# Kernel tuning notes

Measured on AMD Instinct MI355X. Metric: run time of the kernel, lower is better.

## Reference

```python
import jax, jax.numpy as jnp
import numpy as np

SEQ, BS, H, D = 2048, 2, 16, 64


def phi(x):
    # ELU(x / d**0.25) + 1
    return jax.nn.elu(x / (x.shape[-1] ** 0.25)) + 1.0


def setup_inputs() -> dict:
    key = jax.random.key(0)
    ks = jax.random.split(key, 5)
    return {
        "query_layer": jax.random.normal(ks[0], (SEQ, BS, H, D), jnp.float32),
        "key_layer": jax.random.normal(ks[1], (SEQ, BS, H, D), jnp.float32),
        "value_layer": jax.random.normal(ks[2], (SEQ, BS, H, D), jnp.float32),
        "attention_mask": jnp.zeros((BS, 1, SEQ, SEQ), dtype=bool),  # unused by forward
        "phi_k": jax.random.normal(ks[3], (1, H, D, 1), jnp.float32) / 10000.0,
        "phi_kv": jax.random.normal(ks[4], (1, H, D, D), jnp.float32) / 10000.0,
    }


def _ntk_attn(q, k, v, sum_phi_k, sum_phi_kv):
    # q,k,v: [bs,h,n,d]; sum_phi_k: [1,h,d,1]; sum_phi_kv: [1,h,d,d]
    d = q.shape[-1]
    nq, nk = q.shape[-2], k.shape[-2]
    kk = jnp.abs(sum_phi_k)
    Z = sum_phi_kv
    phi_q = phi(q)  # [bs,h,nq,d]
    A = jnp.einsum("bhqd,bhkd->bhqk", q, k) / jnp.sqrt(jnp.float32(d))
    max_A = jnp.max(A, axis=-1, keepdims=True)  # [bs,h,nq,1]
    exp_max_A = jnp.exp(max_A)
    A = jnp.exp(A - max_A)
    causal = jnp.tril(jnp.ones((nq, nk), jnp.float32), k=nk - nq)
    A = A * causal  # broadcast over [bs,h]
    D_norm = jnp.sum(A, axis=-1, keepdims=True) + jnp.matmul(phi_q, kk) / exp_max_A
    ctx = (jnp.matmul(A, v) + jnp.matmul(phi_q, Z) / exp_max_A) / D_norm
    return ctx  # [bs,h,nq,d]


def reference(query_layer, key_layer, value_layer, attention_mask, phi_k, phi_kv):
    # inputs are [seq, bs, h, d]; attention_mask is unused (module ignores it)
    q = jnp.transpose(query_layer, (1, 2, 0, 3)).astype(jnp.float32)
    k = jnp.transpose(key_layer, (1, 2, 0, 3)).astype(jnp.float32)
    v = jnp.transpose(value_layer, (1, 2, 0, 3)).astype(jnp.float32)
    ctx = _ntk_attn(q, k, v, phi_k, phi_kv)  # [bs,h,nq,d]
    ctx = jnp.transpose(ctx, (2, 0, 1, 3))  # [nq,bs,h,d]
    nq, bs, h, d = ctx.shape
    return ctx.reshape(nq, bs, h * d).astype(query_layer.dtype)
```

## Files before the change

### kernel.cpp

```cpp
#include <hip/hip_runtime.h>

#define SEQ 2048
#define BSZ 2
#define NHEAD 16
#define NBH (BSZ * NHEAD)
#define HDIM 64
#define QBLK 64
#define KVBLK 64
#define NQT (SEQ / QBLK)
#define ROWSTRIDE (BSZ * NHEAD * HDIM)

typedef __bf16 bf16x8 __attribute__((ext_vector_type(8)));
typedef __bf16 bf16x4 __attribute__((ext_vector_type(4)));
typedef float f32x4 __attribute__((ext_vector_type(4)));

#define AS1 __attribute__((address_space(1)))
#define AS3 __attribute__((address_space(3)))

__global__ __launch_bounds__(256)
void conv_all(const float* __restrict__ Kg, const float* __restrict__ Vg,
              const float* __restrict__ PKVg, __bf16* __restrict__ Kb,
              __bf16* __restrict__ Vt, __bf16* __restrict__ Ztb) {
  __shared__ __bf16 tt[HDIM][72];
  const int b = blockIdx.x;
  const int tid = threadIdx.x;

  if (b < 2048) {
    const int t = b * 256 + tid;
    const int s = t >> 8;
    const int bh = (t >> 3) & 31;
    const int d8 = (t & 7) * 8;
    const float* src = Kg + (size_t)s * ROWSTRIDE + bh * HDIM + d8;
    const float4 a = *(const float4*)src;
    const float4 bb = *(const float4*)(src + 4);
    bf16x8 o = {(__bf16)a.x, (__bf16)a.y, (__bf16)a.z, (__bf16)a.w,
                (__bf16)bb.x, (__bf16)bb.y, (__bf16)bb.z, (__bf16)bb.w};
    const int slot = (d8 >> 3) ^ (s & 7);
    *(bf16x8*)(Kb + ((size_t)bh * SEQ + s) * HDIM + slot * 8) = o;
  } else if (b < 3072) {
    const int t = b - 2048;
    const int kb = t & 31, bh = t >> 5;
    {
      const int r = tid >> 2, c16 = (tid & 3) * 16;
#pragma unroll
      for (int i = 0; i < 4; ++i) {
        const float4 v = *(const float4*)(Vg + (size_t)(kb * 64 + r) * ROWSTRIDE +
                                          bh * HDIM + c16 + 4 * i);
        tt[c16 + 4 * i + 0][r] = (__bf16)v.x;
        tt[c16 + 4 * i + 1][r] = (__bf16)v.y;
        tt[c16 + 4 * i + 2][r] = (__bf16)v.z;
        tt[c16 + 4 * i + 3][r] = (__bf16)v.w;
      }
    }
    __syncthreads();
    {
      const int d = tid >> 2, c2 = (tid & 3) * 2;
#pragma unroll
      for (int k8 = 0; k8 < 2; ++k8) {
        const int s8 = c2 + k8;
        const int pbase = (s8 ^ (d & 7)) * 8;
        __bf16 ov[8];
#pragma unroll
        for (int j = 0; j < 8; ++j) {
          const int p = pbase + j;
          const int P = p >> 5, g = (p >> 3) & 3, jj = p & 7;
          ov[j] = tt[d][32 * P + 16 * (jj >> 2) + 4 * g + (jj & 3)];
        }
        *(bf16x8*)(Vt + (((size_t)bh * 32 + kb) * 64 + d) * 64 + s8 * 8) =
            *(const bf16x8*)ov;
      }
    }
  } else {
    const int t = (b - 3072) * 256 + tid;
    const int lr = t & 15, lg = (t >> 4) & 3, c = (t >> 6) & 1;
    const int dj = (t >> 7) & 3, h = t >> 9;
    __bf16 o[8];
#pragma unroll
    for (int i = 0; i < 8; ++i)
      o[i] = (__bf16)PKVg[((size_t)h * 64 + 32 * c + 8 * lg + i) * 64 + dj * 16 + lr];
    *(bf16x8*)(Ztb + (size_t)t * 8) = *(const bf16x8*)o;
  }
}

__global__ __launch_bounds__(256, 4)
void ntk_attn(const float* __restrict__ Qg, const __bf16* __restrict__ Kb,
              const __bf16* __restrict__ Vt, const float* __restrict__ PKg,
              const __bf16* __restrict__ Ztb, float* __restrict__ Og) {
  __shared__ __bf16 Ks[2][KVBLK * HDIM];
  __shared__ __bf16 Vts[2][KVBLK * HDIM];

  const int tid = threadIdx.x;
  const int w = tid >> 6, l = tid & 63, lr = l & 15, lg = l >> 4;

  const int ord = blockIdx.x;
  const int bh = ord & 31, h = bh & (NHEAD - 1);
  const int v = ord >> 5;
  const int bx = (v < 16) ? v : 47 - v;
  const int q0 = bx * QBLK;
  const int ntile = bx + 1;
  const int headoff = bh * HDIM;
  const __bf16* Kbh = Kb + (size_t)bh * SEQ * HDIM;
  const __bf16* Vbh = Vt + (size_t)bh * SEQ * HDIM;

  auto stage = [&](int kb, int bb) {
    const char* gk = (const char*)Kbh + ((size_t)kb << 13) + (w << 11) + (l << 4);
    const char* gv = (const char*)Vbh + ((size_t)kb << 13) + (w << 11) + (l << 4);
    __bf16* lk = &Ks[bb][w << 10];
    __bf16* lv = &Vts[bb][w << 10];
    __builtin_amdgcn_global_load_lds((const AS1 unsigned*)gk,
                                     (AS3 unsigned*)lk, 16, 0, 0);
    __builtin_amdgcn_global_load_lds((const AS1 unsigned*)(gk + 1024),
                                     (AS3 unsigned*)(lk + 512), 16, 0, 0);
    __builtin_amdgcn_global_load_lds((const AS1 unsigned*)gv,
                                     (AS3 unsigned*)lv, 16, 0, 0);
    __builtin_amdgcn_global_load_lds((const AS1 unsigned*)(gv + 1024),
                                     (AS3 unsigned*)(lv + 512), 16, 0, 0);
  };

  stage(0, 0);

  bf16x8 aq[2], pq[2];
  {
    const float* qp = Qg + (size_t)(q0 + w * 16 + lr) * ROWSTRIDE + headoff + lg * 8;
#pragma unroll
    for (int c = 0; c < 2; ++c) {
      const float4 x0 = *(const float4*)(qp + 32 * c);
      const float4 x1 = *(const float4*)(qp + 32 * c + 4);
      const float f[8] = {x0.x, x0.y, x0.z, x0.w, x1.x, x1.y, x1.z, x1.w};
#pragma unroll
      for (int i = 0; i < 8; ++i) {
        aq[c][i] = (__bf16)(f[i] * 0.18033688011112042f);
        const float xs = f[i] * 0.3535533905932738f;
        pq[c][i] = (__bf16)(xs > 0.f ? xs + 1.f : __expf(xs));
      }
    }
  }

  const f32x4 z4 = {0.f, 0.f, 0.f, 0.f};
  f32x4 oacc[4] = {z4, z4, z4, z4};
  f32x4 dacc = z4;
  bf16x8 ones;
#pragma unroll
  for (int i = 0; i < 8; ++i) ones[i] = (__bf16)1.0f;
  const int qa = q0 + w * 16 + lr;
  const int sw = lr & 7;

  __syncthreads();
  int cur = 0;

  for (int kb = 0; kb < ntile; ++kb) {
    const bool more = (kb + 1 < ntile);
    if (more) stage(kb + 1, cur ^ 1);

    bf16x8 kc[4][2];
#pragma unroll
    for (int nj = 0; nj < 4; ++nj)
#pragma unroll
      for (int c = 0; c < 2; ++c)
        kc[nj][c] = *(const bf16x8*)&Ks[cur][(nj * 16 + lr) * 64 +
                                            (((4 * c + lg) ^ sw) << 3)];
    bf16x8 vv[2][4];
#pragma unroll
    for (int P = 0; P < 2; ++P)
#pragma unroll
      for (int dj = 0; dj < 4; ++dj)
        vv[P][dj] = *(const bf16x8*)&Vts[cur][(dj * 16 + lr) * 64 +
                                             (((4 * P + lg) ^ sw) << 3)];

    f32x4 s4[4];
#pragma unroll
    for (int nj = 0; nj < 4; ++nj) {
      f32x4 acc = z4;
#pragma unroll
      for (int c = 0; c < 2; ++c)
        acc = __builtin_amdgcn_mfma_f32_16x16x32_bf16(kc[nj][c], aq[c], acc, 0, 0, 0);
      s4[nj] = acc;
    }

    bf16x4 p4[4];
    const bool diag = (kb == bx);
    const int kv0 = kb * KVBLK;
#pragma unroll
    for (int nj = 0; nj < 4; ++nj) {
#pragma unroll
      for (int r = 0; r < 4; ++r) {
        float e;
        if (diag) {
          const int kabs = kv0 + 16 * nj + 4 * lg + r;
          e = (kabs <= qa) ? __builtin_amdgcn_exp2f(s4[nj][r]) : 0.f;
        } else {
          e = __builtin_amdgcn_exp2f(s4[nj][r]);
        }
        p4[nj][r] = (__bf16)e;
      }
    }

#pragma unroll
    for (int P = 0; P < 2; ++P) {
      const bf16x8 pa = __builtin_shufflevector(p4[2 * P], p4[2 * P + 1],
                                                0, 1, 2, 3, 4, 5, 6, 7);
      dacc = __builtin_amdgcn_mfma_f32_16x16x32_bf16(pa, ones, dacc, 0, 0, 0);
#pragma unroll
      for (int dj = 0; dj < 4; ++dj)
        oacc[dj] = __builtin_amdgcn_mfma_f32_16x16x32_bf16(pa, vv[P][dj],
                                                           oacc[dj], 0, 0, 0);
    }

    if (more) {
      __syncthreads();
      cur ^= 1;
    }
  }

  float pkk = 0.f;
  {
#pragma unroll
    for (int c = 0; c < 2; ++c) {
      const float* kp = PKg + h * HDIM + 32 * c + 8 * lg;
      const float4 a = *(const float4*)kp;
      const float4 b = *(const float4*)(kp + 4);
      const float ka[8] = {a.x, a.y, a.z, a.w, b.x, b.y, b.z, b.w};
#pragma unroll
      for (int i = 0; i < 8; ++i)
        pkk += (float)pq[c][i] * fabsf(ka[i]);
    }
    pkk += __shfl_xor(pkk, 16);
    pkk += __shfl_xor(pkk, 32);
  }

  f32x4 zacc[4] = {z4, z4, z4, z4};
  const __bf16* Zf = Ztb + (size_t)h * 4096;
#pragma unroll
  for (int c = 0; c < 2; ++c) {
#pragma unroll
    for (int dj = 0; dj < 4; ++dj) {
      const bf16x8 bz = *(const bf16x8*)(Zf + ((dj * 2 + c) * 64 + l) * 8);
      zacc[dj] = __builtin_amdgcn_mfma_f32_16x16x32_bf16(pq[c], bz, zacc[dj], 0, 0, 0);
    }
  }

#pragma unroll
  for (int r = 0; r < 4; ++r) {
    const float rd = 1.f / (dacc[r] + __shfl(pkk, lg * 4 + r));
    float* op = Og + (size_t)(q0 + w * 16 + lg * 4 + r) * ROWSTRIDE + headoff;
#pragma unroll
    for (int dj = 0; dj < 4; ++dj)
      op[dj * 16 + lr] = (oacc[dj][r] + zacc[dj][r]) * rd;
  }
}

extern "C" void kernel_launch(void* const* d_in, const int* in_sizes, int n_in,
                              void* d_out, int out_size, void* d_ws, size_t ws_size,
                              hipStream_t stream) {
  const float* Qg  = (const float*)d_in[0];
  const float* Kg  = (const float*)d_in[1];
  const float* Vg  = (const float*)d_in[2];
  const float* PKg  = (const float*)d_in[4];
  const float* PKVg = (const float*)d_in[5];
  float* Og = (float*)d_out;

  __bf16* Kb  = (__bf16*)d_ws;
  __bf16* Vt  = Kb + (size_t)NBH * SEQ * HDIM;
  __bf16* Ztb = Vt + (size_t)NBH * SEQ * HDIM;

  conv_all<<<dim3(2048 + 1024 + 32), dim3(256), 0, stream>>>(Kg, Vg, PKVg,
                                                             Kb, Vt, Ztb);
  ntk_attn<<<dim3(NQT * NBH), dim3(256), 0, stream>>>(Qg, Kb, Vt, PKg, Ztb, Og);
}
```

Before: 45.94 us.

## Split waves 2x2 over query and KV halves with LDS reduction

Each wave now handles 32 query rows against half of each KV tile, where before it handled 16 query rows against the full tile. Partial output and denominator accumulators are reduced across wave pairs through LDS at the end. The goal is to cut per-wave LDS reads of K and V fragments, since each fragment is now reused across two query chunks. In exchange it adds an extra synchronisation and LDS reduction phase, raises register pressure from the doubled accumulators, and leaves half the waves idle during the final store.

```diff
diff --git a/kernel.cpp b/kernel.cpp
--- a/kernel.cpp
+++ b/kernel.cpp
@@ -91,6 +91,8 @@
 
   const int tid = threadIdx.x;
   const int w = tid >> 6, l = tid & 63, lr = l & 15, lg = l >> 4;
+  const int qh = w >> 1;
+  const int kvh = w & 1;
 
   const int ord = blockIdx.x;
   const int bh = ord & 31, h = bh & (NHEAD - 1);
@@ -119,9 +121,13 @@
 
   stage(0, 0);
 
-  bf16x8 aq[2], pq[2];
-  {
-    const float* qp = Qg + (size_t)(q0 + w * 16 + lr) * ROWSTRIDE + headoff + lg * 8;
+  bf16x8 aq[2][2], pq[2][2];
+  int qa[2];
+#pragma unroll
+  for (int qc = 0; qc < 2; ++qc) {
+    const int qrow = q0 + 32 * qh + 16 * qc + lr;
+    qa[qc] = qrow;
+    const float* qp = Qg + (size_t)qrow * ROWSTRIDE + headoff + lg * 8;
 #pragma unroll
     for (int c = 0; c < 2; ++c) {
       const float4 x0 = *(const float4*)(qp + 32 * c);
@@ -129,20 +135,19 @@
       const float f[8] = {x0.x, x0.y, x0.z, x0.w, x1.x, x1.y, x1.z, x1.w};
 #pragma unroll
       for (int i = 0; i < 8; ++i) {
-        aq[c][i] = (__bf16)(f[i] * 0.18033688011112042f);
+        aq[qc][c][i] = (__bf16)(f[i] * 0.18033688011112042f);
         const float xs = f[i] * 0.3535533905932738f;
-        pq[c][i] = (__bf16)(xs > 0.f ? xs + 1.f : __expf(xs));
+        pq[qc][c][i] = (__bf16)(xs > 0.f ? xs + 1.f : __expf(xs));
       }
     }
   }
 
   const f32x4 z4 = {0.f, 0.f, 0.f, 0.f};
-  f32x4 oacc[4] = {z4, z4, z4, z4};
-  f32x4 dacc = z4;
+  f32x4 oacc[2][4] = {{z4, z4, z4, z4}, {z4, z4, z4, z4}};
+  f32x4 dacc[2] = {z4, z4};
   bf16x8 ones;
 #pragma unroll
   for (int i = 0; i < 8; ++i) ones[i] = (__bf16)1.0f;
-  const int qa = q0 + w * 16 + lr;
   const int sw = lr & 7;
 
   __syncthreads();
@@ -152,58 +157,55 @@
     const bool more = (kb + 1 < ntile);
     if (more) stage(kb + 1, cur ^ 1);
 
-    bf16x8 kc[4][2];
-#pragma unroll
-    for (int nj = 0; nj < 4; ++nj)
+    bf16x8 kc[2][2];
+#pragma unroll
+    for (int nj = 0; nj < 2; ++nj)
 #pragma unroll
       for (int c = 0; c < 2; ++c)
-        kc[nj][c] = *(const bf16x8*)&Ks[cur][(nj * 16 + lr) * 64 +
+        kc[nj][c] = *(const bf16x8*)&Ks[cur][(32 * kvh + nj * 16 + lr) * 64 +
                                             (((4 * c + lg) ^ sw) << 3)];
-    bf16x8 vv[2][4];
-#pragma unroll
-    for (int P = 0; P < 2; ++P)
+    bf16x8 vv[4];
+#pragma unroll
+    for (int dj = 0; dj < 4; ++dj)
+      vv[dj] = *(const bf16x8*)&Vts[cur][(dj * 16 + lr) * 64 +
+                                         (((4 * kvh + lg) ^ sw) << 3)];
+
+    const bool diag = (kb == bx);
+    const int kvbase = kb * KVBLK + 32 * kvh;
+#pragma unroll
+    for (int qc = 0; qc < 2; ++qc) {
+      f32x4 s4[2];
+#pragma unroll
+      for (int nj = 0; nj < 2; ++nj) {
+        f32x4 acc = z4;
+        acc = __builtin_amdgcn_mfma_f32_16x16x32_bf16(kc[nj][0], aq[qc][0], acc, 0, 0, 0);
+        acc = __builtin_amdgcn_mfma_f32_16x16x32_bf16(kc[nj][1], aq[qc][1], acc, 0, 0, 0);
+        s4[nj] = acc;
+      }
+
+      bf16x4 p4[2];
+#pragma unroll
+      for (int nj = 0; nj < 2; ++nj) {
+#pragma unroll
+        for (int r = 0; r < 4; ++r) {
+          float e;
+          if (diag) {
+            const int kabs = kvbase + 16 * nj + 4 * lg + r;
+            e = (kabs <= qa[qc]) ? __builtin_amdgcn_exp2f(s4[nj][r]) : 0.f;
+          } else {
+            e = __builtin_amdgcn_exp2f(s4[nj][r]);
+          }
+          p4[nj][r] = (__bf16)e;
+        }
+      }
+
+      const bf16x8 pa = __builtin_shufflevector(p4[0], p4[1],
+                                                0, 1, 2, 3, 4, 5, 6, 7);
+      dacc[qc] = __builtin_amdgcn_mfma_f32_16x16x32_bf16(pa, ones, dacc[qc], 0, 0, 0);
 #pragma unroll
       for (int dj = 0; dj < 4; ++dj)
-        vv[P][dj] = *(const bf16x8*)&Vts[cur][(dj * 16 + lr) * 64 +
-                                             (((4 * P + lg) ^ sw) << 3)];
-
-    f32x4 s4[4];
-#pragma unroll
-    for (int nj = 0; nj < 4; ++nj) {
-      f32x4 acc = z4;
-#pragma unroll
-      for (int c = 0; c < 2; ++c)
-        acc = __builtin_amdgcn_mfma_f32_16x16x32_bf16(kc[nj][c], aq[c], acc, 0, 0, 0);
-      s4[nj] = acc;
-    }
-
-    bf16x4 p4[4];
-    const bool diag = (kb == bx);
-    const int kv0 = kb * KVBLK;
-#pragma unroll
-    for (int nj = 0; nj < 4; ++nj) {
-#pragma unroll
-      for (int r = 0; r < 4; ++r) {
-        float e;
-        if (diag) {
-          const int kabs = kv0 + 16 * nj + 4 * lg + r;
-          e = (kabs <= qa) ? __builtin_amdgcn_exp2f(s4[nj][r]) : 0.f;
-        } else {
-          e = __builtin_amdgcn_exp2f(s4[nj][r]);
-        }
-        p4[nj][r] = (__bf16)e;
-      }
-    }
-
-#pragma unroll
-    for (int P = 0; P < 2; ++P) {
-      const bf16x8 pa = __builtin_shufflevector(p4[2 * P], p4[2 * P + 1],
-                                                0, 1, 2, 3, 4, 5, 6, 7);
-      dacc = __builtin_amdgcn_mfma_f32_16x16x32_bf16(pa, ones, dacc, 0, 0, 0);
-#pragma unroll
-      for (int dj = 0; dj < 4; ++dj)
-        oacc[dj] = __builtin_amdgcn_mfma_f32_16x16x32_bf16(pa, vv[P][dj],
-                                                           oacc[dj], 0, 0, 0);
+        oacc[qc][dj] = __builtin_amdgcn_mfma_f32_16x16x32_bf16(pa, vv[dj],
+                                                              oacc[qc][dj], 0, 0, 0);
     }
 
     if (more) {
@@ -212,40 +214,68 @@
     }
   }
 
-  float pkk = 0.f;
-  {
-#pragma unroll
-    for (int c = 0; c < 2; ++c) {
-      const float* kp = PKg + h * HDIM + 32 * c + 8 * lg;
-      const float4 a = *(const float4*)kp;
-      const float4 b = *(const float4*)(kp + 4);
-      const float ka[8] = {a.x, a.y, a.z, a.w, b.x, b.y, b.z, b.w};
-#pragma unroll
-      for (int i = 0; i < 8; ++i)
-        pkk += (float)pq[c][i] * fabsf(ka[i]);
-    }
-    pkk += __shfl_xor(pkk, 16);
-    pkk += __shfl_xor(pkk, 32);
-  }
-
-  f32x4 zacc[4] = {z4, z4, z4, z4};
+  __syncthreads();
+  float* XO = (float*)&Ks[0][0];
+  float* XD = (float*)&Vts[0][0];
   const __bf16* Zf = Ztb + (size_t)h * 4096;
-#pragma unroll
-  for (int c = 0; c < 2; ++c) {
-#pragma unroll
-    for (int dj = 0; dj < 4; ++dj) {
-      const bf16x8 bz = *(const bf16x8*)(Zf + ((dj * 2 + c) * 64 + l) * 8);
-      zacc[dj] = __builtin_amdgcn_mfma_f32_16x16x32_bf16(pq[c], bz, zacc[dj], 0, 0, 0);
-    }
-  }
-
-#pragma unroll
-  for (int r = 0; r < 4; ++r) {
-    const float rd = 1.f / (dacc[r] + __shfl(pkk, lg * 4 + r));
-    float* op = Og + (size_t)(q0 + w * 16 + lg * 4 + r) * ROWSTRIDE + headoff;
-#pragma unroll
-    for (int dj = 0; dj < 4; ++dj)
-      op[dj * 16 + lr] = (oacc[dj][r] + zacc[dj][r]) * rd;
+  float pkk[2] = {0.f, 0.f};
+
+  if (kvh == 1) {
+#pragma unroll
+    for (int qc = 0; qc < 2; ++qc)
+#pragma unroll
+      for (int c = 0; c < 2; ++c)
+#pragma unroll
+        for (int dj = 0; dj < 4; ++dj) {
+          const bf16x8 bz = *(const bf16x8*)(Zf + ((dj * 2 + c) * 64 + l) * 8);
+          oacc[qc][dj] = __builtin_amdgcn_mfma_f32_16x16x32_bf16(pq[qc][c], bz,
+                                                                oacc[qc][dj], 0, 0, 0);
+        }
+#pragma unroll
+    for (int qc = 0; qc < 2; ++qc) {
+#pragma unroll
+      for (int dj = 0; dj < 4; ++dj)
+        *(f32x4*)&XO[(((qh * 2 + qc) * 4 + dj) * 64 + l) * 4] = oacc[qc][dj];
+      *(f32x4*)&XD[((qh * 2 + qc) * 64 + l) * 4] = dacc[qc];
+    }
+  } else {
+#pragma unroll
+    for (int qc = 0; qc < 2; ++qc) {
+      float p = 0.f;
+#pragma unroll
+      for (int c = 0; c < 2; ++c) {
+        const float* kp = PKg + h * HDIM + 32 * c + 8 * lg;
+        const float4 a = *(const float4*)kp;
+        const float4 b = *(const float4*)(kp + 4);
+        const float ka[8] = {a.x, a.y, a.z, a.w, b.x, b.y, b.z, b.w};
+#pragma unroll
+        for (int i = 0; i < 8; ++i)
+          p += (float)pq[qc][c][i] * fabsf(ka[i]);
+      }
+      p += __shfl_xor(p, 16);
+      p += __shfl_xor(p, 32);
+      pkk[qc] = p;
+    }
+  }
+  __syncthreads();
+
+  if (kvh == 0) {
+#pragma unroll
+    for (int qc = 0; qc < 2; ++qc) {
+#pragma unroll
+      for (int dj = 0; dj < 4; ++dj)
+        oacc[qc][dj] += *(const f32x4*)&XO[(((qh * 2 + qc) * 4 + dj) * 64 + l) * 4];
+      dacc[qc] += *(const f32x4*)&XD[((qh * 2 + qc) * 64 + l) * 4];
+#pragma unroll
+      for (int r = 0; r < 4; ++r) {
+        const float rd = 1.f / (dacc[qc][r] + __shfl(pkk[qc], lg * 4 + r));
+        float* op = Og + (size_t)(q0 + 32 * qh + 16 * qc + 4 * lg + r) * ROWSTRIDE +
+                    headoff;
+#pragma unroll
+        for (int dj = 0; dj < 4; ++dj)
+          op[dj * 16 + lr] = oacc[qc][dj][r] * rd;
+      }
+    }
   }
 }
 
```

After: 49.24 us. 7.2% more time.
